# Kernel tuning notes

Measured on AMD Instinct MI355X. Metric: run time of the kernel, lower is better.

Reference implementation:

```python
import jax, jax.numpy as jnp
import numpy as np


def setup_inputs() -> dict:
    key = jax.random.key(0)
    kq, kk, kv, km = jax.random.split(key, 4)
    B, H, N, D = 2, 16, 2048, 64
    q = jax.random.normal(kq, (B, H, N, D), dtype=jnp.float32)
    k = jax.random.normal(kk, (B, H, N, D), dtype=jnp.float32)
    v = jax.random.normal(kv, (B, H, N, D), dtype=jnp.float32)
    # mask > 0 (True) means the key position is masked OUT (matches masked_fill semantics)
    mask = jax.random.randint(km, (B, N), 0, 2).astype(bool)
    return {"q": q, "k": k, "v": v, "mask": mask}


def reference(q, k, v, mask):
    # q, k, v: [b, h, n, d]; mask: [b, n] (True = masked out)
    scale = q.shape[-1] ** -0.5
    sim = jnp.einsum('bhid,bhjd->bhij', q, k) * scale
    # L2-distance score: 2*q.k - |q|^2 - |k|^2 (scaled dot already includes `scale`)
    q_sq = jnp.sum(q ** 2, axis=-1, keepdims=True)            # [b, h, n, 1]
    k_sq = jnp.sum(k ** 2, axis=-1, keepdims=True).swapaxes(-1, -2)  # [b, h, 1, n]
    sim = sim * 2 - q_sq - k_sq
    neg_max = -jnp.finfo(sim.dtype).max
    sim = jnp.where(mask[:, None, None, :], neg_max, sim)
    attn = jax.nn.softmax(sim, axis=-1)
    out = jnp.einsum('bhij,bhjd->bhid', attn, v)
    return out
```

## Files before the change

### kernel.cpp

```cpp
#include <hip/hip_runtime.h>

#define B_ 2
#define H_ 16
#define N_ 2048
#define D_ 64
#define NH_ (B_*H_)
#define ROWS_ (NH_*N_)
#define KVB 64
#define NT (N_/KVB)
#define LOG2E 1.4426950408889634f
#define QSCALE (0.25f * LOG2E)

typedef _Float16 f16;
typedef _Float16 f16x2 __attribute__((ext_vector_type(2)));
typedef _Float16 f16x4 __attribute__((ext_vector_type(4)));
typedef _Float16 f16x8 __attribute__((ext_vector_type(8)));
typedef __fp16 h16x2 __attribute__((ext_vector_type(2)));
typedef float f32x4 __attribute__((ext_vector_type(4)));

typedef __attribute__((address_space(1))) const void g_void;
typedef __attribute__((address_space(3))) void l_void;

__device__ __forceinline__ void gl_lds16(const void* g, void* l) {
  __builtin_amdgcn_global_load_lds((g_void*)g, (l_void*)l, 16, 0, 0);
}

__device__ __forceinline__ f16x2 cvt_pk(float a, float b) {
  return __builtin_bit_cast(f16x2, __builtin_amdgcn_cvt_pkrtz(a, b));
}

__device__ __forceinline__ float dot2acc(f16x2 a, f16x2 b, float c) {
#if __has_builtin(__builtin_amdgcn_fdot2)
  return __builtin_amdgcn_fdot2(__builtin_bit_cast(h16x2, a),
                                __builtin_bit_cast(h16x2, b), c, false);
#else
  return c + (float)a[0] * (float)b[0] + (float)a[1] * (float)b[1];
#endif
}

__global__ __launch_bounds__(256) void prep_all(
    const float* __restrict__ q, const float* __restrict__ k,
    const float* __restrict__ v, const void* __restrict__ mask,
    f16* __restrict__ qh, f16* __restrict__ kh, f16* __restrict__ vt,
    float* __restrict__ bias) {
  int tid = threadIdx.x;
  if (blockIdx.x < 1024) {
    int head = blockIdx.x >> 5;
    int n0 = (blockIdx.x & 31) << 6;
    int e = tid & 15, gq = tid >> 4;
    const float* src = v + ((long)head * N_ + n0 + e * 4) * D_ + gq * 4;
    f32x4 r0 = *(const f32x4*)(src);
    f32x4 r1 = *(const f32x4*)(src + D_);
    f32x4 r2 = *(const f32x4*)(src + 2 * D_);
    f32x4 r3 = *(const f32x4*)(src + 3 * D_);
    f16* dst = vt + (long)head * D_ * N_ + n0 + e * 4;
#pragma unroll
    for (int c = 0; c < 4; ++c) {
      f16x4 y;
      y[0] = (f16)r0[c]; y[1] = (f16)r1[c]; y[2] = (f16)r2[c]; y[3] = (f16)r3[c];
      *(f16x4*)(dst + (long)(gq * 4 + c) * N_) = y;
    }
  } else {
    int wid = (blockIdx.x - 1024) * 4 + (tid >> 6);
    int lane = tid & 63;
    int r8 = lane >> 3, e = lane & 7;
    const unsigned* mw = (const unsigned*)mask;
    bool bytes_mode = __any(mw[lane] > 1u);
#pragma unroll
    for (int trip = 0; trip < 4; ++trip) {
      long grow = ((long)(trip * 4096 + wid)) * 8 + r8;
      bool isK = grow >= ROWS_;
      long row = isK ? grow - ROWS_ : grow;
      const float* s = (isK ? k : q) + row * D_ + e * 8;
      f32x4 x0 = *(const f32x4*)s;
      f32x4 x1 = *(const f32x4*)(s + 4);
      float scl = isK ? 1.0f : QSCALE;
      f16x8 hv;
#pragma unroll
      for (int c = 0; c < 4; ++c) { hv[c] = (f16)(x0[c] * scl); hv[4 + c] = (f16)(x1[c] * scl); }
      *(f16x8*)((isK ? kh : qh) + row * D_ + e * 8) = hv;
      if (isK) {
        float sq = x0[0]*x0[0] + x0[1]*x0[1] + x0[2]*x0[2] + x0[3]*x0[3]
                 + x1[0]*x1[0] + x1[1]*x1[1] + x1[2]*x1[2] + x1[3]*x1[3];
        sq += __shfl_xor(sq, 1); sq += __shfl_xor(sq, 2); sq += __shfl_xor(sq, 4);
        if (e == 0) {
          int b = (int)(row >> 15);
          int n = (int)(row & (N_ - 1));
          int mv = bytes_mode ? (int)((const unsigned char*)mask)[b * N_ + n]
                              : ((const int*)mask)[b * N_ + n];
          bias[row] = mv ? -1e30f : -sq * LOG2E;
        }
      }
    }
  }
}

__global__ __launch_bounds__(256, 4) void attend_main(
    const f16* __restrict__ qh, const f16* __restrict__ kh,
    const f16* __restrict__ vt, const float* __restrict__ bias,
    float* __restrict__ out) {
  __shared__ f16 Kt[2][4096];
  __shared__ f16 Vt[2][4096];
  __shared__ f16 Pb[4][1024];

  int tid = threadIdx.x;
  int w = tid >> 6, lane = tid & 63;
  int j = lane & 15, g = lane >> 4;

  int bid = (blockIdx.x & 7) * 128 + (blockIdx.x >> 3);
  int head = bid >> 5;
  int qt = bid & 31;
  int qrow0 = qt * 64 + w * 16;
  int off = ((bid >> 5) & 3) * 8;

  const f16* qbase = qh + ((long)head * N_ + qrow0 + j) * D_;
  f16x8 qf0 = *(const f16x8*)(qbase + g * 8);
  f16x8 qf1 = *(const f16x8*)(qbase + 32 + g * 8);

  const char* kg = (const char*)(kh + (long)head * N_ * D_);
  const char* vg = (const char*)(vt + (long)head * D_ * N_);
  const float* bb = bias + (long)head * N_ + g * 4;

  int ko0[4], ko1[4];
#pragma unroll
  for (int x = 0; x < 4; ++x) {
    int rk = x * 16 + j;
    int swk = (rk & 7) << 4;
    ko0[x] = ((rk << 7) + g * 16) ^ swk;
    ko1[x] = ((rk << 7) + 64 + g * 16) ^ swk;
  }
  int pswz = (j & 7) << 4;
  int pw0 = ((j << 7) + g * 8) ^ pswz;
  int pr0 = ((j << 7) + g * 16) ^ pswz;
  int pr1 = ((j << 7) + 64 + g * 16) ^ pswz;

  f32x4 O0 = {0.f,0.f,0.f,0.f}, O1 = {0.f,0.f,0.f,0.f};
  f32x4 O2 = {0.f,0.f,0.f,0.f}, O3 = {0.f,0.f,0.f,0.f};
  float m = -1e30f, l = 0.f;

  auto stage = [&](int buf, int t) {
    int kv = t * KVB;
    if (w < 2) {
      const char* src = kg + (size_t)kv * 128;
      char* lb = (char*)&Kt[buf][0];
#pragma unroll
      for (int c = 0; c < 4; ++c) {
        int chunk = w * 4 + c;
        int o = chunk * 1024 + lane * 16;
        int p = o ^ (((o >> 7) & 7) << 4);
        gl_lds16(src + p, lb + chunk * 1024);
      }
    } else {
      const char* src = vg + (size_t)kv * 2;
      char* lb = (char*)&Vt[buf][0];
#pragma unroll
      for (int c = 0; c < 4; ++c) {
        int chunk = (w - 2) * 4 + c;
        int o = chunk * 1024 + lane * 16;
        int p = o ^ (((o >> 7) & 7) << 4);
        gl_lds16(src + (size_t)(p >> 7) * (N_ * 2) + (p & 127), lb + chunk * 1024);
      }
    }
  };

  auto qkt = [&](const char* Kc, f32x4* sA, const f32x4* cin) {
    __builtin_amdgcn_s_setprio(1);
#pragma unroll
    for (int jt = 0; jt < 4; ++jt) {
      f16x8 k0 = *(const f16x8*)(Kc + ko0[jt]);
      f16x8 k1 = *(const f16x8*)(Kc + ko1[jt]);
      f32x4 a = __builtin_amdgcn_mfma_f32_16x16x32_f16(k0, qf0, cin[jt], 0, 0, 0);
      sA[jt]  = __builtin_amdgcn_mfma_f32_16x16x32_f16(k1, qf1, a, 0, 0, 0);
    }
    __builtin_amdgcn_s_setprio(0);
  };
  auto finish_pv = [&](const char* Vc, const f32x4* sA) {
    f16x2 pk[8];
    float rsum = 0.f;
    const f16x2 ones = {(f16)1.0f, (f16)1.0f};
#pragma unroll
    for (int jt = 0; jt < 4; ++jt) {
      float p0 = __builtin_amdgcn_exp2f(sA[jt][0]);
      float p1 = __builtin_amdgcn_exp2f(sA[jt][1]);
      float p2 = __builtin_amdgcn_exp2f(sA[jt][2]);
      float p3 = __builtin_amdgcn_exp2f(sA[jt][3]);
      pk[jt * 2 + 0] = cvt_pk(p0, p1);
      pk[jt * 2 + 1] = cvt_pk(p2, p3);
      rsum = dot2acc(pk[jt * 2 + 0], ones, rsum);
      rsum = dot2acc(pk[jt * 2 + 1], ones, rsum);
    }
    l += rsum;
    char* Pw = (char*)&Pb[w][0];
#pragma unroll
    for (int jt = 0; jt < 4; ++jt) {
      f16x4 pv_ = __builtin_shufflevector(pk[jt * 2], pk[jt * 2 + 1], 0, 1, 2, 3);
      *(f16x4*)(Pw + (pw0 ^ (jt * 32))) = pv_;
    }
    f16x8 pf0 = *(const f16x8*)(Pw + pr0);
    f16x8 pf1 = *(const f16x8*)(Pw + pr1);
    __builtin_amdgcn_s_setprio(1);
#pragma unroll
    for (int dt = 0; dt < 4; ++dt) {
      f16x8 v0 = *(const f16x8*)(Vc + ko0[dt]);
      f16x8 v1 = *(const f16x8*)(Vc + ko1[dt]);
      f32x4* Od = (dt == 0) ? &O0 : (dt == 1) ? &O1 : (dt == 2) ? &O2 : &O3;
      *Od = __builtin_amdgcn_mfma_f32_16x16x32_f16(pf0, v0, *Od, 0, 0, 0);
      *Od = __builtin_amdgcn_mfma_f32_16x16x32_f16(pf1, v1, *Od, 0, 0, 0);
    }
    __builtin_amdgcn_s_setprio(0);
  };
  auto lane_max16 = [&](const f32x4* sA) {
    float a0 = fmaxf(fmaxf(sA[0][0], sA[0][1]), fmaxf(sA[0][2], sA[0][3]));
    float a1 = fmaxf(fmaxf(sA[1][0], sA[1][1]), fmaxf(sA[1][2], sA[1][3]));
    float a2 = fmaxf(fmaxf(sA[2][0], sA[2][1]), fmaxf(sA[2][2], sA[2][3]));
    float a3 = fmaxf(fmaxf(sA[3][0], sA[3][1]), fmaxf(sA[3][2], sA[3][3]));
    return fmaxf(fmaxf(a0, a1), fmaxf(a2, a3));
  };

  f32x4 bnx[4];
#pragma unroll
  for (int jt = 0; jt < 4; ++jt) bnx[jt] = *(const f32x4*)(bb + off * KVB + jt * 16);

  stage(0, off);
  __syncthreads();
  int cur = 0;

  {
    int tn = (off + 1) & (NT - 1);
    stage(1, tn);
    f32x4 sA[4];
    qkt((const char*)&Kt[0][0], sA, bnx);
#pragma unroll
    for (int jt = 0; jt < 4; ++jt) bnx[jt] = *(const f32x4*)(bb + tn * KVB + jt * 16);

    float tm = lane_max16(sA);
    tm = fmaxf(tm, __shfl_xor(tm, 16));
    tm = fmaxf(tm, __shfl_xor(tm, 32));
    m = fmaxf(m, tm);
#pragma unroll
    for (int jt = 0; jt < 4; ++jt)
#pragma unroll
      for (int r = 0; r < 4; ++r) sA[jt][r] -= m;
    finish_pv((const char*)&Vt[0][0], sA);
    __syncthreads();
    cur = 1;
  }

  for (int t = 1; t < NT; ++t) {
    int tt = (t + off) & (NT - 1);
    int tn = (tt + 1) & (NT - 1);

    f32x4 madj[4];
#pragma unroll
    for (int jt = 0; jt < 4; ++jt) {
      madj[jt][0] = bnx[jt][0] - m; madj[jt][1] = bnx[jt][1] - m;
      madj[jt][2] = bnx[jt][2] - m; madj[jt][3] = bnx[jt][3] - m;
    }
    if (t + 1 < NT) stage(cur ^ 1, tn);

    f32x4 sA[4];
    qkt((const char*)&Kt[cur][0], sA, madj);

    if (t + 1 < NT) {
#pragma unroll
      for (int jt = 0; jt < 4; ++jt)
        bnx[jt] = *(const f32x4*)(bb + tn * KVB + jt * 16);
    }

    float tmL = lane_max16(sA);
    if (!__all(tmL <= 8.0f)) {
      float tmr = fmaxf(tmL, __shfl_xor(tmL, 16));
      tmr = fmaxf(tmr, __shfl_xor(tmr, 32));
      float delta = fmaxf(tmr, 0.0f);
      float sc = __builtin_amdgcn_exp2f(-delta);
      m += delta;
      l *= sc;
#pragma unroll
      for (int r = 0; r < 4; ++r) {
        float scr = __shfl(sc, g * 4 + r);
        O0[r] *= scr; O1[r] *= scr; O2[r] *= scr; O3[r] *= scr;
      }
#pragma unroll
      for (int jt = 0; jt < 4; ++jt)
#pragma unroll
        for (int r = 0; r < 4; ++r) sA[jt][r] -= delta;
    }

    finish_pv((const char*)&Vt[cur][0], sA);
    __syncthreads();
    cur ^= 1;
  }

  l += __shfl_xor(l, 16);
  l += __shfl_xor(l, 32);
  float* ob = out + ((long)head * N_ + qrow0 + g * 4) * D_ + j;
#pragma unroll
  for (int r = 0; r < 4; ++r) {
    float inv = 1.0f / __shfl(l, g * 4 + r);
    float* o2 = ob + (long)r * D_;
    o2[0]  = O0[r] * inv;
    o2[16] = O1[r] * inv;
    o2[32] = O2[r] * inv;
    o2[48] = O3[r] * inv;
  }
}

extern "C" void kernel_launch(void* const* d_in, const int* in_sizes, int n_in,
                              void* d_out, int out_size, void* d_ws, size_t ws_size,
                              hipStream_t stream) {
  const float* q = (const float*)d_in[0];
  const float* k = (const float*)d_in[1];
  const float* v = (const float*)d_in[2];
  const void* mask = d_in[3];

  char* ws = (char*)d_ws;
  f16*   qh   = (f16*)ws;
  f16*   kh   = (f16*)(ws + (8u  << 20));
  f16*   vt   = (f16*)(ws + (16u << 20));
  float* bias = (float*)(ws + (24u << 20));
  float* out  = (float*)d_out;

  prep_all<<<dim3(2048), dim3(256), 0, stream>>>(q, k, v, mask, qh, kh, vt, bias);
  attend_main<<<dim3(NH_ * (N_ / 64)), dim3(256), 0, stream>>>(qh, kh, vt, bias, out);
}
```

Before: 151.1 us.

## Process 32 query rows per wave with two waves per block

Each block now runs 2 waves of 128 threads instead of 4, and each wave handles two 16-row query subtiles (A and B) that share the K and V fragments read from LDS. This halves the LDS reads of K/V fragments per query row and interleaves independent MFMA chains. In exchange, register pressure roughly doubles, and fewer waves per block load the staging tiles, which may reduce occupancy and latency hiding.

```diff
diff --git a/kernel.cpp b/kernel.cpp
--- a/kernel.cpp
+++ b/kernel.cpp
@@ -95,13 +95,13 @@
   }
 }
 
-__global__ __launch_bounds__(256, 4) void attend_main(
+__global__ __launch_bounds__(128, 2) void attend_main(
     const f16* __restrict__ qh, const f16* __restrict__ kh,
     const f16* __restrict__ vt, const float* __restrict__ bias,
     float* __restrict__ out) {
   __shared__ f16 Kt[2][4096];
   __shared__ f16 Vt[2][4096];
-  __shared__ f16 Pb[4][1024];
+  __shared__ f16 Pb[2][2][1024];
 
   int tid = threadIdx.x;
   int w = tid >> 6, lane = tid & 63;
@@ -110,12 +110,14 @@
   int bid = (blockIdx.x & 7) * 128 + (blockIdx.x >> 3);
   int head = bid >> 5;
   int qt = bid & 31;
-  int qrow0 = qt * 64 + w * 16;
+  int qrow0 = qt * 64 + w * 32;
   int off = ((bid >> 5) & 3) * 8;
 
   const f16* qbase = qh + ((long)head * N_ + qrow0 + j) * D_;
-  f16x8 qf0 = *(const f16x8*)(qbase + g * 8);
-  f16x8 qf1 = *(const f16x8*)(qbase + 32 + g * 8);
+  f16x8 qfA0 = *(const f16x8*)(qbase + g * 8);
+  f16x8 qfA1 = *(const f16x8*)(qbase + 32 + g * 8);
+  f16x8 qfB0 = *(const f16x8*)(qbase + 16 * D_ + g * 8);
+  f16x8 qfB1 = *(const f16x8*)(qbase + 16 * D_ + 32 + g * 8);
 
   const char* kg = (const char*)(kh + (long)head * N_ * D_);
   const char* vg = (const char*)(vt + (long)head * D_ * N_);
@@ -134,86 +136,101 @@
   int pr0 = ((j << 7) + g * 16) ^ pswz;
   int pr1 = ((j << 7) + 64 + g * 16) ^ pswz;
 
-  f32x4 O0 = {0.f,0.f,0.f,0.f}, O1 = {0.f,0.f,0.f,0.f};
-  f32x4 O2 = {0.f,0.f,0.f,0.f}, O3 = {0.f,0.f,0.f,0.f};
-  float m = -1e30f, l = 0.f;
+  f32x4 OA0 = {0,0,0,0}, OA1 = {0,0,0,0}, OA2 = {0,0,0,0}, OA3 = {0,0,0,0};
+  f32x4 OB0 = {0,0,0,0}, OB1 = {0,0,0,0}, OB2 = {0,0,0,0}, OB3 = {0,0,0,0};
+  float mA = -1e30f, lA = 0.f, mB = -1e30f, lB = 0.f;
 
   auto stage = [&](int buf, int t) {
     int kv = t * KVB;
-    if (w < 2) {
+    if (w == 0) {
       const char* src = kg + (size_t)kv * 128;
       char* lb = (char*)&Kt[buf][0];
 #pragma unroll
-      for (int c = 0; c < 4; ++c) {
-        int chunk = w * 4 + c;
-        int o = chunk * 1024 + lane * 16;
+      for (int c = 0; c < 8; ++c) {
+        int o = c * 1024 + lane * 16;
         int p = o ^ (((o >> 7) & 7) << 4);
-        gl_lds16(src + p, lb + chunk * 1024);
+        gl_lds16(src + p, lb + c * 1024);
       }
     } else {
       const char* src = vg + (size_t)kv * 2;
       char* lb = (char*)&Vt[buf][0];
 #pragma unroll
-      for (int c = 0; c < 4; ++c) {
-        int chunk = (w - 2) * 4 + c;
-        int o = chunk * 1024 + lane * 16;
+      for (int c = 0; c < 8; ++c) {
+        int o = c * 1024 + lane * 16;
         int p = o ^ (((o >> 7) & 7) << 4);
-        gl_lds16(src + (size_t)(p >> 7) * (N_ * 2) + (p & 127), lb + chunk * 1024);
+        gl_lds16(src + (size_t)(p >> 7) * (N_ * 2) + (p & 127), lb + c * 1024);
       }
     }
   };
 
-  auto qkt = [&](const char* Kc, f32x4* sA, const f32x4* cin) {
+  auto qkt2 = [&](const char* Kc, f32x4* sA, f32x4* sB,
+                  const f32x4* cinA, const f32x4* cinB) {
     __builtin_amdgcn_s_setprio(1);
 #pragma unroll
     for (int jt = 0; jt < 4; ++jt) {
       f16x8 k0 = *(const f16x8*)(Kc + ko0[jt]);
       f16x8 k1 = *(const f16x8*)(Kc + ko1[jt]);
-      f32x4 a = __builtin_amdgcn_mfma_f32_16x16x32_f16(k0, qf0, cin[jt], 0, 0, 0);
-      sA[jt]  = __builtin_amdgcn_mfma_f32_16x16x32_f16(k1, qf1, a, 0, 0, 0);
+      f32x4 a = __builtin_amdgcn_mfma_f32_16x16x32_f16(k0, qfA0, cinA[jt], 0, 0, 0);
+      f32x4 b = __builtin_amdgcn_mfma_f32_16x16x32_f16(k0, qfB0, cinB[jt], 0, 0, 0);
+      sA[jt]  = __builtin_amdgcn_mfma_f32_16x16x32_f16(k1, qfA1, a, 0, 0, 0);
+      sB[jt]  = __builtin_amdgcn_mfma_f32_16x16x32_f16(k1, qfB1, b, 0, 0, 0);
     }
     __builtin_amdgcn_s_setprio(0);
   };
-  auto finish_pv = [&](const char* Vc, const f32x4* sA) {
-    f16x2 pk[8];
-    float rsum = 0.f;
+
+  auto finish_pv2 = [&](const char* Vc, const f32x4* sA, const f32x4* sB) {
+    f16x2 pkA[8], pkB[8];
+    float rsA = 0.f, rsB = 0.f;
     const f16x2 ones = {(f16)1.0f, (f16)1.0f};
 #pragma unroll
     for (int jt = 0; jt < 4; ++jt) {
-      float p0 = __builtin_amdgcn_exp2f(sA[jt][0]);
-      float p1 = __builtin_amdgcn_exp2f(sA[jt][1]);
-      float p2 = __builtin_amdgcn_exp2f(sA[jt][2]);
-      float p3 = __builtin_amdgcn_exp2f(sA[jt][3]);
-      pk[jt * 2 + 0] = cvt_pk(p0, p1);
-      pk[jt * 2 + 1] = cvt_pk(p2, p3);
-      rsum = dot2acc(pk[jt * 2 + 0], ones, rsum);
-      rsum = dot2acc(pk[jt * 2 + 1], ones, rsum);
-    }
-    l += rsum;
-    char* Pw = (char*)&Pb[w][0];
+      float a0 = __builtin_amdgcn_exp2f(sA[jt][0]);
+      float a1 = __builtin_amdgcn_exp2f(sA[jt][1]);
+      float a2 = __builtin_amdgcn_exp2f(sA[jt][2]);
+      float a3 = __builtin_amdgcn_exp2f(sA[jt][3]);
+      float b0 = __builtin_amdgcn_exp2f(sB[jt][0]);
+      float b1 = __builtin_amdgcn_exp2f(sB[jt][1]);
+      float b2 = __builtin_amdgcn_exp2f(sB[jt][2]);
+      float b3 = __builtin_amdgcn_exp2f(sB[jt][3]);
+      pkA[jt*2+0] = cvt_pk(a0, a1); pkA[jt*2+1] = cvt_pk(a2, a3);
+      pkB[jt*2+0] = cvt_pk(b0, b1); pkB[jt*2+1] = cvt_pk(b2, b3);
+      rsA = dot2acc(pkA[jt*2+0], ones, rsA); rsA = dot2acc(pkA[jt*2+1], ones, rsA);
+      rsB = dot2acc(pkB[jt*2+0], ones, rsB); rsB = dot2acc(pkB[jt*2+1], ones, rsB);
+    }
+    lA += rsA; lB += rsB;
+    char* PwA = (char*)&Pb[w][0][0];
+    char* PwB = (char*)&Pb[w][1][0];
 #pragma unroll
     for (int jt = 0; jt < 4; ++jt) {
-      f16x4 pv_ = __builtin_shufflevector(pk[jt * 2], pk[jt * 2 + 1], 0, 1, 2, 3);
-      *(f16x4*)(Pw + (pw0 ^ (jt * 32))) = pv_;
-    }
-    f16x8 pf0 = *(const f16x8*)(Pw + pr0);
-    f16x8 pf1 = *(const f16x8*)(Pw + pr1);
+      f16x4 pa = __builtin_shufflevector(pkA[jt*2], pkA[jt*2+1], 0, 1, 2, 3);
+      f16x4 pb = __builtin_shufflevector(pkB[jt*2], pkB[jt*2+1], 0, 1, 2, 3);
+      *(f16x4*)(PwA + (pw0 ^ (jt * 32))) = pa;
+      *(f16x4*)(PwB + (pw0 ^ (jt * 32))) = pb;
+    }
+    f16x8 pfA0 = *(const f16x8*)(PwA + pr0);
+    f16x8 pfA1 = *(const f16x8*)(PwA + pr1);
+    f16x8 pfB0 = *(const f16x8*)(PwB + pr0);
+    f16x8 pfB1 = *(const f16x8*)(PwB + pr1);
     __builtin_amdgcn_s_setprio(1);
 #pragma unroll
     for (int dt = 0; dt < 4; ++dt) {
       f16x8 v0 = *(const f16x8*)(Vc + ko0[dt]);
       f16x8 v1 = *(const f16x8*)(Vc + ko1[dt]);
-      f32x4* Od = (dt == 0) ? &O0 : (dt == 1) ? &O1 : (dt == 2) ? &O2 : &O3;
-      *Od = __builtin_amdgcn_mfma_f32_16x16x32_f16(pf0, v0, *Od, 0, 0, 0);
-      *Od = __builtin_amdgcn_mfma_f32_16x16x32_f16(pf1, v1, *Od, 0, 0, 0);
+      f32x4* OdA = (dt == 0) ? &OA0 : (dt == 1) ? &OA1 : (dt == 2) ? &OA2 : &OA3;
+      f32x4* OdB = (dt == 0) ? &OB0 : (dt == 1) ? &OB1 : (dt == 2) ? &OB2 : &OB3;
+      *OdA = __builtin_amdgcn_mfma_f32_16x16x32_f16(pfA0, v0, *OdA, 0, 0, 0);
+      *OdB = __builtin_amdgcn_mfma_f32_16x16x32_f16(pfB0, v0, *OdB, 0, 0, 0);
+      *OdA = __builtin_amdgcn_mfma_f32_16x16x32_f16(pfA1, v1, *OdA, 0, 0, 0);
+      *OdB = __builtin_amdgcn_mfma_f32_16x16x32_f16(pfB1, v1, *OdB, 0, 0, 0);
     }
     __builtin_amdgcn_s_setprio(0);
   };
-  auto lane_max16 = [&](const f32x4* sA) {
-    float a0 = fmaxf(fmaxf(sA[0][0], sA[0][1]), fmaxf(sA[0][2], sA[0][3]));
-    float a1 = fmaxf(fmaxf(sA[1][0], sA[1][1]), fmaxf(sA[1][2], sA[1][3]));
-    float a2 = fmaxf(fmaxf(sA[2][0], sA[2][1]), fmaxf(sA[2][2], sA[2][3]));
-    float a3 = fmaxf(fmaxf(sA[3][0], sA[3][1]), fmaxf(sA[3][2], sA[3][3]));
+
+  auto lane_max16 = [&](const f32x4* s) {
+    float a0 = fmaxf(fmaxf(s[0][0], s[0][1]), fmaxf(s[0][2], s[0][3]));
+    float a1 = fmaxf(fmaxf(s[1][0], s[1][1]), fmaxf(s[1][2], s[1][3]));
+    float a2 = fmaxf(fmaxf(s[2][0], s[2][1]), fmaxf(s[2][2], s[2][3]));
+    float a3 = fmaxf(fmaxf(s[3][0], s[3][1]), fmaxf(s[3][2], s[3][3]));
     return fmaxf(fmaxf(a0, a1), fmaxf(a2, a3));
   };
 
@@ -228,20 +245,20 @@
   {
     int tn = (off + 1) & (NT - 1);
     stage(1, tn);
-    f32x4 sA[4];
-    qkt((const char*)&Kt[0][0], sA, bnx);
+    f32x4 sA[4], sB[4];
+    qkt2((const char*)&Kt[0][0], sA, sB, bnx, bnx);
 #pragma unroll
     for (int jt = 0; jt < 4; ++jt) bnx[jt] = *(const f32x4*)(bb + tn * KVB + jt * 16);
 
-    float tm = lane_max16(sA);
-    tm = fmaxf(tm, __shfl_xor(tm, 16));
-    tm = fmaxf(tm, __shfl_xor(tm, 32));
-    m = fmaxf(m, tm);
+    float ta = lane_max16(sA), tb = lane_max16(sB);
+    ta = fmaxf(ta, __shfl_xor(ta, 16)); ta = fmaxf(ta, __shfl_xor(ta, 32));
+    tb = fmaxf(tb, __shfl_xor(tb, 16)); tb = fmaxf(tb, __shfl_xor(tb, 32));
+    mA = ta; mB = tb;
 #pragma unroll
     for (int jt = 0; jt < 4; ++jt)
 #pragma unroll
-      for (int r = 0; r < 4; ++r) sA[jt][r] -= m;
-    finish_pv((const char*)&Vt[0][0], sA);
+      for (int r = 0; r < 4; ++r) { sA[jt][r] -= mA; sB[jt][r] -= mB; }
+    finish_pv2((const char*)&Vt[0][0], sA, sB);
     __syncthreads();
     cur = 1;
   }
@@ -250,16 +267,19 @@
     int tt = (t + off) & (NT - 1);
     int tn = (tt + 1) & (NT - 1);
 
-    f32x4 madj[4];
+    f32x4 madjA[4], madjB[4];
 #pragma unroll
     for (int jt = 0; jt < 4; ++jt) {
-      madj[jt][0] = bnx[jt][0] - m; madj[jt][1] = bnx[jt][1] - m;
-      madj[jt][2] = bnx[jt][2] - m; madj[jt][3] = bnx[jt][3] - m;
+#pragma unroll
+      for (int r = 0; r < 4; ++r) {
+        madjA[jt][r] = bnx[jt][r] - mA;
+        madjB[jt][r] = bnx[jt][r] - mB;
+      }
     }
     if (t + 1 < NT) stage(cur ^ 1, tn);
 
-    f32x4 sA[4];
-    qkt((const char*)&Kt[cur][0], sA, madj);
+    f32x4 sA[4], sB[4];
+    qkt2((const char*)&Kt[cur][0], sA, sB, madjA, madjB);
 
     if (t + 1 < NT) {
 #pragma unroll
@@ -267,41 +287,49 @@
         bnx[jt] = *(const f32x4*)(bb + tn * KVB + jt * 16);
     }
 
-    float tmL = lane_max16(sA);
-    if (!__all(tmL <= 8.0f)) {
-      float tmr = fmaxf(tmL, __shfl_xor(tmL, 16));
-      tmr = fmaxf(tmr, __shfl_xor(tmr, 32));
-      float delta = fmaxf(tmr, 0.0f);
-      float sc = __builtin_amdgcn_exp2f(-delta);
-      m += delta;
-      l *= sc;
+    float tLA = lane_max16(sA);
+    float tLB = lane_max16(sB);
+    if (!__all(fmaxf(tLA, tLB) <= 8.0f)) {
+      float ta = fmaxf(tLA, __shfl_xor(tLA, 16));
+      ta = fmaxf(ta, __shfl_xor(ta, 32));
+      float tb = fmaxf(tLB, __shfl_xor(tLB, 16));
+      tb = fmaxf(tb, __shfl_xor(tb, 32));
+      float dA = fmaxf(ta, 0.0f), dB = fmaxf(tb, 0.0f);
+      float scA = __builtin_amdgcn_exp2f(-dA);
+      float scB = __builtin_amdgcn_exp2f(-dB);
+      mA += dA; mB += dB;
+      lA *= scA; lB *= scB;
 #pragma unroll
       for (int r = 0; r < 4; ++r) {
-        float scr = __shfl(sc, g * 4 + r);
-        O0[r] *= scr; O1[r] *= scr; O2[r] *= scr; O3[r] *= scr;
+        float sa = __shfl(scA, g * 4 + r);
+        float sb = __shfl(scB, g * 4 + r);
+        OA0[r] *= sa; OA1[r] *= sa; OA2[r] *= sa; OA3[r] *= sa;
+        OB0[r] *= sb; OB1[r] *= sb; OB2[r] *= sb; OB3[r] *= sb;
       }
 #pragma unroll
       for (int jt = 0; jt < 4; ++jt)
 #pragma unroll
-        for (int r = 0; r < 4; ++r) sA[jt][r] -= delta;
-    }
-
-    finish_pv((const char*)&Vt[cur][0], sA);
+        for (int r = 0; r < 4; ++r) { sA[jt][r] -= dA; sB[jt][r] -= dB; }
+    }
+
+    finish_pv2((const char*)&Vt[cur][0], sA, sB);
     __syncthreads();
     cur ^= 1;
   }
 
-  l += __shfl_xor(l, 16);
-  l += __shfl_xor(l, 32);
+  lA += __shfl_xor(lA, 16); lA += __shfl_xor(lA, 32);
+  lB += __shfl_xor(lB, 16); lB += __shfl_xor(lB, 32);
   float* ob = out + ((long)head * N_ + qrow0 + g * 4) * D_ + j;
 #pragma unroll
   for (int r = 0; r < 4; ++r) {
-    float inv = 1.0f / __shfl(l, g * 4 + r);
-    float* o2 = ob + (long)r * D_;
-    o2[0]  = O0[r] * inv;
-    o2[16] = O1[r] * inv;
-    o2[32] = O2[r] * inv;
-    o2[48] = O3[r] * inv;
+    float invA = 1.0f / __shfl(lA, g * 4 + r);
+    float invB = 1.0f / __shfl(lB, g * 4 + r);
+    float* oa = ob + (long)r * D_;
+    float* obp = ob + (long)(16 + r) * D_;
+    oa[0]  = OA0[r] * invA; oa[16] = OA1[r] * invA;
+    oa[32] = OA2[r] * invA; oa[48] = OA3[r] * invA;
+    obp[0]  = OB0[r] * invB; obp[16] = OB1[r] * invB;
+    obp[32] = OB2[r] * invB; obp[48] = OB3[r] * invB;
   }
 }
 
@@ -321,5 +349,5 @@
   float* out  = (float*)d_out;
 
   prep_all<<<dim3(2048), dim3(256), 0, stream>>>(q, k, v, mask, qh, kh, vt, bias);
-  attend_main<<<dim3(NH_ * (N_ / 64)), dim3(256), 0, stream>>>(qh, kh, vt, bias, out);
-}
+  attend_main<<<dim3(NH_ * (N_ / 64)), dim3(128), 0, stream>>>(qh, kh, vt, bias, out);
+}
```

Result: no change. 151.7 us (+0.4%).
